# Optimization experiments

Measured on AMD Instinct MI355X. Metric: run time of the kernel, lower is better.

The kernel has to match this reference:

```python
import jax, jax.numpy as jnp
import numpy as np
from jax import lax

N_STATES = 128
N_NL = 64
N_IN = 64
N_OUT = 32
N_SYS = 16
FILT = 24
GAMMA = 1e-3
Q_VAL = 10.0
BETA = 1e5
EPS = 1e-3
BATCH = 131072


def setup_inputs() -> dict:
    key = jax.random.key(0)
    ks = jax.random.split(key, 11)
    std = 0.1
    return {
        "inpt": jax.random.normal(ks[0], (BATCH, N_IN), jnp.float32),
        "state": jax.random.normal(ks[1], (BATCH, N_STATES), jnp.float32),
        "X": jax.random.normal(ks[2], (2 * N_STATES + N_NL, 2 * N_STATES + N_NL), jnp.float32) * std,
        "Y1": jax.random.normal(ks[3], (N_STATES, N_STATES), jnp.float32) * std,
        "X3": jax.random.normal(ks[4], (N_OUT, N_OUT), jnp.float32) * std,
        "Y3": jax.random.normal(ks[5], (N_OUT, N_OUT), jnp.float32) * std,
        "Z3": jax.random.normal(ks[6], (abs(N_IN - N_OUT), N_OUT), jnp.float32) * std,
        "B2": jax.random.normal(ks[7], (N_STATES, N_IN), jnp.float32) * std,
        "C2": jax.random.normal(ks[8], (N_OUT, N_STATES), jnp.float32) * std,
        "D21": jax.random.normal(ks[9], (N_OUT, N_NL), jnp.float32) * std,
        "D12": jax.random.normal(ks[10], (N_NL, N_IN), jnp.float32) * std,
    }


def _derived(X, Y1, X3, Y3, Z3, B2, C2, D21, D12):
    # set_model_param(): build contracting REN matrices from free params.
    s = min(N_IN, N_OUT)  # = N_OUT here
    Q = -Q_VAL * jnp.eye(N_OUT, dtype=X.dtype)
    m = N_IN - N_SYS
    R_diag = jnp.concatenate([
        BETA * jnp.ones(N_SYS), GAMMA * jnp.ones(FILT - 1),
        jnp.array([BETA]), GAMMA * jnp.ones(m - FILT)]).astype(X.dtype)
    R = jnp.diag(R_diag)
    I_s = jnp.eye(s, dtype=X.dtype)
    M = X3.T @ X3 + Y3 - Y3.T + Z3.T @ Z3 + EPS * I_s
    Minv = jnp.linalg.inv(I_s + M)
    # n_outputs < n_inputs branch
    N = jnp.concatenate([Minv @ (I_s - M), -2.0 * Minv @ Z3.T], axis=1)  # [n_out, n_in]
    Lq = jnp.linalg.cholesky(-Q).T
    Lr = jnp.linalg.cholesky(R).T
    D22 = jnp.linalg.inv(Lq) @ N @ Lr  # [n_out, n_in]
    R_cal = R + D22.T @ Q @ D22
    R_cal_inv = jnp.linalg.inv(R_cal)
    C2_cal = (D22.T @ Q @ C2).T            # [n_states, n_in]
    D21_cal = (D22.T @ Q @ D21).T - D12    # [n_nl, n_in]
    vec_r = jnp.concatenate([C2_cal, D21_cal, B2], axis=0)
    psi_r = vec_r @ R_cal_inv @ vec_r.T
    vec_q = jnp.concatenate([C2.T, D21.T, jnp.zeros((N_STATES, N_OUT), X.dtype)], axis=0)
    psi_q = vec_q @ Q @ vec_q.T
    n = 2 * N_STATES + N_NL
    H = X.T @ X + EPS * jnp.eye(n, dtype=X.dtype) + psi_r - psi_q
    ns, nl = N_STATES, N_NL
    H11 = H[:ns, :ns]
    H21 = H[ns:ns + nl, :ns]
    H22 = H[ns:ns + nl, ns:ns + nl]
    H31 = H[ns + nl:, :ns]
    H32 = H[ns + nl:, ns:ns + nl]
    H33 = H[ns + nl:, ns + nl:]
    Fm = H31
    B1 = H32
    E = 0.5 * (H11 + H33 + Y1 - Y1.T)
    Lam = 0.5 * jnp.diag(H22)
    D11 = -jnp.tril(H22, k=-1)  # strictly lower triangular
    C1 = -H21
    return Fm, B1, E, Lam, C1, D11, D22


def _ren_forward(inpt, state, X, Y1, X3, Y3, Z3, B2, C2, D21, D12):
    Fm, B1, E, Lam, C1, D11, D22 = _derived(X, Y1, X3, Y3, Z3, B2, C2, D21, D12)
    B = state.shape[0]
    # precompute the state/input contribution to every nonlinearity row
    a = state @ C1.T + inpt @ D12.T  # [B, n_nl] (bias = 0, bias=False)

    def step(w, xs):
        i, a_col, d11_row, lam = xs
        v = a_col + w @ d11_row                 # forward substitution: D11 strictly lower
        w = w.at[:, i].set(jnp.tanh(v / lam))
        return w, None

    w0 = jnp.zeros((B, N_NL), dtype=state.dtype)
    xs = (jnp.arange(N_NL), a.T, D11, Lam)
    w, _ = lax.scan(step, w0, xs)

    E_x_ = state @ Fm.T + w @ B1.T + inpt @ B2.T
    state_plus = E_x_ @ jnp.linalg.inv(E).T
    output = state @ C2.T + w @ D21.T + inpt @ D22.T
    return output, state_plus


def reference(inpt, state, X, Y1, X3, Y3, Z3, B2, C2, D21, D12):
    return _ren_forward(inpt, state, X, Y1, X3, Y3, Z3, B2, C2, D21, D12)
```

## Files before the change

### kernel.cpp

```cpp
#include <hip/hip_runtime.h>
#include <math.h>

#define BATCH 131072
#define NTOT 320

typedef __attribute__((ext_vector_type(8))) short short8;
typedef __attribute__((ext_vector_type(4))) float f32x4;

#define WS_D22   0
#define WS_VR    2048
#define WS_T     22528
#define WS_H     43008
#define WS_E     145408
#define WS_EINV  161792
#define WS_WEXT  178176
#define WS_D11   210944
#define WS_ILAM  215040
#define WS_BFU   215104
#define U_WATH 0
#define U_WATL 16384
#define U_WOT  32768
#define U_WSPH 40960
#define U_WSPL 73728
#define WS_M    (WS_H)
#define WS_A32M (WS_H + 1024)
#define WS_RC   (WS_H + 2048)

__device__ inline unsigned short f2bf(float x){
    unsigned u = __builtin_bit_cast(unsigned, x);
    u += 0x7FFFu + ((u >> 16) & 1u);
    return (unsigned short)(u >> 16);
}
__device__ inline float bf2f(unsigned short h){
    unsigned u = ((unsigned)h) << 16;
    return __builtin_bit_cast(float, u);
}
__device__ inline float r_diag(int j) {
    return (j < 16 || j == 39) ? 100000.0f : 0.001f;
}

__global__ __launch_bounds__(256) void k_der1a(
    const float* __restrict__ X3, const float* __restrict__ Y3,
    const float* __restrict__ Z3, float* __restrict__ ws)
{
    int idx = blockIdx.x*256 + threadIdx.x;
    if (idx >= 1024) return;
    int i = idx >> 5, j = idx & 31;
    float s = 0.f;
    for (int k = 0; k < 32; ++k)
        s += X3[k*32+i]*X3[k*32+j] + Z3[k*32+i]*Z3[k*32+j];
    s += Y3[i*32+j] - Y3[j*32+i];
    if (i == j) s += 0.001f;
    ws[WS_M + idx]    = s;
    ws[WS_A32M + idx] = s + (i == j ? 1.f : 0.f);
}

__global__ __launch_bounds__(1024) void k_gj32(float* __restrict__ ws)
{
    __shared__ float A32[32*33];
    const int t = threadIdx.x;
    const int i = t >> 5, j = t & 31;
    A32[i*33+j] = ws[WS_A32M + i*32 + j];
    __syncthreads();
    for (int k = 0; k < 32; ++k) {
        float ip = 1.f / A32[k*33+k];
        float f  = A32[i*33+k];
        float pj = A32[k*33+j];
        __syncthreads();
        float nv;
        if (i == k) nv = (j == k) ? ip : pj*ip;
        else        nv = (j == k) ? (-f*ip) : (A32[i*33+j] - f*ip*pj);
        A32[i*33+j] = nv;
        __syncthreads();
    }
    ws[WS_A32M + i*32 + j] = A32[i*33+j];
}

__global__ __launch_bounds__(512) void k_der1b(
    const float* __restrict__ Z3, float* __restrict__ ws)
{
    __shared__ float Ms[1024], Mi[1024], D22s[2048];
    const int t = threadIdx.x;
    for (int idx = t; idx < 1024; idx += 512) {
        Ms[idx] = ws[WS_M + idx];
        Mi[idx] = ws[WS_A32M + idx];
    }
    __syncthreads();
    for (int idx = t; idx < 2048; idx += 512) {
        int i = idx >> 6, j = idx & 63;
        float s = 0.f;
        if (j < 32) {
            for (int k = 0; k < 32; ++k) {
                float im = (k == j ? 1.f : 0.f) - Ms[k*32+j];
                s += Mi[i*32+k]*im;
            }
        } else {
            int jj = j - 32;
            for (int k = 0; k < 32; ++k) s += Mi[i*32+k]*Z3[jj*32+k];
            s *= -2.f;
        }
        float d22 = s * sqrtf(r_diag(j)) * 0.31622776601683794f;
        D22s[idx] = d22;
        ws[WS_D22 + idx] = d22;
    }
    __syncthreads();
    for (int idx = t; idx < 4096; idx += 512) {
        int i = idx >> 6, j = idx & 63;
        float s = 0.f;
        for (int k = 0; k < 32; ++k) s += D22s[k*64+i]*D22s[k*64+j];
        float v = -10.f*s;
        if (i == j) v += r_diag(i);
        ws[WS_RC + idx] = v;
    }
}

__global__ __launch_bounds__(256) void k_gj64(float* __restrict__ ws)
{
    __shared__ float piv[2][64];
    __shared__ float fcol[2][64];
    __shared__ float ipd[2];
    const int t = threadIdx.x;
    const int q = t >> 6;
    const int i = t & 63;
    const int c0 = q*16;

    float Ar[16];
    {
        const float* Rin = ws + WS_RC + i*64 + c0;
        #pragma unroll
        for (int jj = 0; jj < 4; ++jj) {
            float4 v = *(const float4*)(Rin + jj*4);
            Ar[jj*4+0]=v.x; Ar[jj*4+1]=v.y; Ar[jj*4+2]=v.z; Ar[jj*4+3]=v.w;
        }
    }

    for (int k = 0; k < 64; ++k) {
        const int b  = k & 1;
        const int kq = k >> 4;
        const int kj = k & 15;

        float f_own = Ar[0];
        #pragma unroll
        for (int jj = 1; jj < 16; ++jj) f_own = (jj == kj) ? Ar[jj] : f_own;

        if (q == kq) fcol[b][i] = f_own;
        if (i == k) {
            #pragma unroll
            for (int jj = 0; jj < 4; ++jj) {
                float4 v;
                v.x = Ar[jj*4+0] + ((q==kq && jj*4+0==kj) ? 1.f : 0.f);
                v.y = Ar[jj*4+1] + ((q==kq && jj*4+1==kj) ? 1.f : 0.f);
                v.z = Ar[jj*4+2] + ((q==kq && jj*4+2==kj) ? 1.f : 0.f);
                v.w = Ar[jj*4+3] + ((q==kq && jj*4+3==kj) ? 1.f : 0.f);
                *(float4*)(&piv[b][c0 + jj*4]) = v;
            }
            if (q == kq) ipd[b] = 1.f / f_own;
        }
        __syncthreads();

        const float ipv = ipd[b];
        if (i == k) {
            #pragma unroll
            for (int jj = 0; jj < 16; ++jj)
                Ar[jj] = (q==kq && jj==kj) ? ipv : Ar[jj]*ipv;
        } else {
            const float g = fcol[b][i] * ipv;
            #pragma unroll
            for (int jj = 0; jj < 4; ++jj) {
                float4 pv = *(const float4*)(&piv[b][c0 + jj*4]);
                Ar[jj*4+0] -= g*pv.x;
                Ar[jj*4+1] -= g*pv.y;
                Ar[jj*4+2] -= g*pv.z;
                Ar[jj*4+3] -= g*pv.w;
            }
        }
    }

    {
        float* Rout = ws + WS_RC + i*64 + c0;
        #pragma unroll
        for (int jj = 0; jj < 4; ++jj) {
            float4 v;
            v.x=Ar[jj*4+0]; v.y=Ar[jj*4+1]; v.z=Ar[jj*4+2]; v.w=Ar[jj*4+3];
            *(float4*)(Rout + jj*4) = v;
        }
    }
}

__global__ __launch_bounds__(256) void k_vecr(
    const float* __restrict__ B2, const float* __restrict__ C2,
    const float* __restrict__ D21, const float* __restrict__ D12,
    float* __restrict__ ws)
{
    int idx = blockIdx.x*256 + threadIdx.x;
    if (idx >= 320*64) return;
    int i = idx >> 6, j = idx & 63;
    const float* D22 = ws + WS_D22;
    float v;
    if (i < 128) {
        float s = 0.f;
        for (int k = 0; k < 32; ++k) s += C2[k*128+i]*D22[k*64+j];
        v = -10.f*s;
    } else if (i < 192) {
        int ii = i - 128;
        float s = 0.f;
        for (int k = 0; k < 32; ++k) s += D21[k*64+ii]*D22[k*64+j];
        v = -10.f*s - D12[ii*64+j];
    } else {
        v = B2[(i-192)*64 + j];
    }
    ws[WS_VR+idx] = v;
}

__global__ __launch_bounds__(256) void k_T(float* __restrict__ ws)
{
    int idx = blockIdx.x*256 + threadIdx.x;
    if (idx >= 320*64) return;
    int i = idx >> 6, j = idx & 63;
    const float* VR = ws + WS_VR + i*64;
    const float* RC = ws + WS_RC;
    float s = 0.f;
    for (int k = 0; k < 64; ++k) s += VR[k] * RC[k*64+j];
    ws[WS_T+idx] = s;
}

__global__ void k_H(const float* __restrict__ X, const float* __restrict__ C2,
                    const float* __restrict__ D21, float* __restrict__ ws)
{
    int idx = blockIdx.x*256 + threadIdx.x;
    if (idx >= NTOT*NTOT) return;
    int i = idx / NTOT, j = idx % NTOT;
    float s = (i == j) ? 0.001f : 0.f;
    for (int k = 0; k < NTOT; ++k) s += X[k*NTOT+i]*X[k*NTOT+j];
    const float* T  = ws + WS_T;
    const float* vr = ws + WS_VR;
    float s2 = 0.f;
    for (int k = 0; k < 64; ++k) s2 += T[i*64+k]*vr[j*64+k];
    s += s2;
    if (i < 192 && j < 192) {
        float s3 = 0.f;
        for (int k = 0; k < 32; ++k) {
            float qi = (i < 128) ? C2[k*128+i] : D21[k*64 + (i-128)];
            float qj = (j < 128) ? C2[k*128+j] : D21[k*64 + (j-128)];
            s3 += qi*qj;
        }
        s += 10.f*s3;
    }
    ws[WS_H + idx] = s;
}

__global__ void k_extract(const float* __restrict__ Y1, const float* __restrict__ C2,
                          const float* __restrict__ D21, const float* __restrict__ D12,
                          const float* __restrict__ B2, float* __restrict__ ws)
{
    const float* H = ws + WS_H;
    unsigned short* bfb = (unsigned short*)(ws + WS_BFU);
    int tid = blockIdx.x*blockDim.x + threadIdx.x;
    int nth = gridDim.x*blockDim.x;
    for (int idx = tid; idx < 128*128; idx += nth) {
        int i = idx >> 7, j = idx & 127;
        ws[WS_E+idx] = 0.5f*(H[i*320+j] + H[(192+i)*320 + 192+j] + Y1[i*128+j] - Y1[j*128+i]);
    }
    for (int i = tid; i < 64; i += nth)
        ws[WS_ILAM+i] = 2.0f / H[(128+i)*320 + 128+i];
    for (int idx = tid; idx < 64*64; idx += nth) {
        int i = idx >> 6, j = idx & 63;
        ws[WS_D11+idx] = (j < i) ? -H[(128+i)*320 + 128+j] : 0.f;
    }
    for (int idx = tid; idx < 128*256; idx += nth) {
        int m = idx >> 8, k = idx & 255;
        ws[WS_WEXT+idx] = (k < 192) ? H[(192+m)*320 + k] : B2[m*64 + (k-192)];
    }
    for (int idx = tid; idx < 64*256; idx += nth) {
        int j = idx >> 8, k = idx & 255;
        float v;
        if (k < 128)      v = -H[(128+j)*320 + k];
        else if (k < 192) v = 0.f;
        else              v = D12[j*64 + (k-192)];
        unsigned short hi = f2bf(v);
        bfb[U_WATH+idx] = hi;
        bfb[U_WATL+idx] = f2bf(v - bf2f(hi));
    }
    const float* D22 = ws + WS_D22;
    for (int idx = tid; idx < 32*256; idx += nth) {
        int c = idx >> 8, k = idx & 255;
        float v;
        if (k < 128)      v = C2[c*128+k];
        else if (k < 192) v = D21[c*64 + (k-128)];
        else              v = D22[c*64 + (k-192)];
        bfb[U_WOT+idx] = f2bf(v);
    }
}

__global__ __launch_bounds__(1024) void k_inv128(float* __restrict__ ws)
{
    __shared__ float piv[2][128];
    __shared__ float fcol[2][128];
    __shared__ float ipd[2];
    const int t = threadIdx.x;
    const int q = t >> 7;
    const int i = t & 127;
    const int c0 = q*16;

    float Ar[16];
    {
        const float* Ein = ws + WS_E + i*128 + c0;
        #pragma unroll
        for (int jj = 0; jj < 4; ++jj) {
            float4 v = *(const float4*)(Ein + jj*4);
            Ar[jj*4+0]=v.x; Ar[jj*4+1]=v.y; Ar[jj*4+2]=v.z; Ar[jj*4+3]=v.w;
        }
    }

    for (int k = 0; k < 128; ++k) {
        const int b  = k & 1;
        const int kq = k >> 4;
        const int kj = k & 15;

        float f_own = Ar[0];
        #pragma unroll
        for (int jj = 1; jj < 16; ++jj) f_own = (jj == kj) ? Ar[jj] : f_own;

        if (q == kq) fcol[b][i] = f_own;
        if (i == k) {
            #pragma unroll
            for (int jj = 0; jj < 4; ++jj) {
                float4 v;
                v.x = Ar[jj*4+0] + ((q==kq && jj*4+0==kj) ? 1.f : 0.f);
                v.y = Ar[jj*4+1] + ((q==kq && jj*4+1==kj) ? 1.f : 0.f);
                v.z = Ar[jj*4+2] + ((q==kq && jj*4+2==kj) ? 1.f : 0.f);
                v.w = Ar[jj*4+3] + ((q==kq && jj*4+3==kj) ? 1.f : 0.f);
                *(float4*)(&piv[b][c0 + jj*4]) = v;
            }
            if (q == kq) ipd[b] = 1.f / f_own;
        }
        __syncthreads();

        const float ipv = ipd[b];
        if (i == k) {
            #pragma unroll
            for (int jj = 0; jj < 16; ++jj)
                Ar[jj] = (q==kq && jj==kj) ? ipv : Ar[jj]*ipv;
        } else {
            const float g = fcol[b][i] * ipv;
            #pragma unroll
            for (int jj = 0; jj < 4; ++jj) {
                float4 pv = *(const float4*)(&piv[b][c0 + jj*4]);
                Ar[jj*4+0] -= g*pv.x;
                Ar[jj*4+1] -= g*pv.y;
                Ar[jj*4+2] -= g*pv.z;
                Ar[jj*4+3] -= g*pv.w;
            }
        }
    }

    {
        float* Eout = ws + WS_EINV + i*128 + c0;
        #pragma unroll
        for (int jj = 0; jj < 4; ++jj) {
            float4 v;
            v.x=Ar[jj*4+0]; v.y=Ar[jj*4+1]; v.z=Ar[jj*4+2]; v.w=Ar[jj*4+3];
            *(float4*)(Eout + jj*4) = v;
        }
    }
}

__global__ __launch_bounds__(256) void k_Wsp(float* __restrict__ ws)
{
    int i = blockIdx.x;
    int k = threadIdx.x;
    const float* Einv = ws + WS_EINV + i*128;
    const float* WexT = ws + WS_WEXT;
    unsigned short* bfb = (unsigned short*)(ws + WS_BFU);
    float s = 0.f;
    for (int m = 0; m < 128; ++m) s += Einv[m] * WexT[m*256 + k];
    unsigned short hi = f2bf(s);
    bfb[U_WSPH + i*256 + k] = hi;
    bfb[U_WSPL + i*256 + k] = f2bf(s - bf2f(hi));
}

__global__ __launch_bounds__(256, 4) void k_batch(
    const float* __restrict__ inpt, const float* __restrict__ state,
    const float* __restrict__ ws, float* __restrict__ out)
{
    __shared__ unsigned short zsh[64*256];
    __shared__ unsigned short D11t[64*64];
    const int t = threadIdx.x;
    const int row0 = blockIdx.x * 64;
    const unsigned short* bfb = (const unsigned short*)(ws + WS_BFU);

    for (int idx = t; idx < 64*16; idx += 256) {
        int r = idx >> 4, c = idx & 15;
        const float4* p = (const float4*)(state + (size_t)(row0+r)*128 + c*8);
        float4 f0 = p[0], f1 = p[1];
        short8 h;
        h[0]=(short)f2bf(f0.x); h[1]=(short)f2bf(f0.y); h[2]=(short)f2bf(f0.z); h[3]=(short)f2bf(f0.w);
        h[4]=(short)f2bf(f1.x); h[5]=(short)f2bf(f1.y); h[6]=(short)f2bf(f1.z); h[7]=(short)f2bf(f1.w);
        *(short8*)(&zsh[r*256 + ((c ^ (r&7)) << 3)]) = h;
    }
    for (int idx = t; idx < 64*8; idx += 256) {
        int r = idx >> 3, cl = idx & 7, c = 24 + cl;
        const float4* p = (const float4*)(inpt + (size_t)(row0+r)*64 + cl*8);
        float4 f0 = p[0], f1 = p[1];
        short8 h;
        h[0]=(short)f2bf(f0.x); h[1]=(short)f2bf(f0.y); h[2]=(short)f2bf(f0.z); h[3]=(short)f2bf(f0.w);
        h[4]=(short)f2bf(f1.x); h[5]=(short)f2bf(f1.y); h[6]=(short)f2bf(f1.z); h[7]=(short)f2bf(f1.w);
        *(short8*)(&zsh[r*256 + ((c ^ (r&7)) << 3)]) = h;
    }
    for (int idx = t; idx < 4096; idx += 256) {
        int j = idx >> 6, i = idx & 63;
        float v = (i == j) ? ws[WS_ILAM + j] : ws[WS_D11 + i*64 + j];
        D11t[idx] = f2bf(v);
    }
    __syncthreads();

    const int wv = t >> 6, lane = t & 63, lr = lane & 15, lk = lane >> 4;

    {
        const unsigned short* WATH = bfb + U_WATH;
        const unsigned short* WATL = bfb + U_WATL;
        f32x4 acc1[4] = {};
        const int ks1[6] = {0,1,2,3,6,7};
        #pragma unroll
        for (int s = 0; s < 6; ++s) {
            int ks = ks1[s];
            short8 bh = *(const short8*)(&WATH[(wv*16+lr)*256 + ks*32 + lk*8]);
            short8 bl = *(const short8*)(&WATL[(wv*16+lr)*256 + ks*32 + lk*8]);
            #pragma unroll
            for (int rt = 0; rt < 4; ++rt) {
                int row = rt*16 + lr, c = ks*4 + lk;
                short8 a = *(const short8*)(&zsh[row*256 + ((c ^ (row&7)) << 3)]);
                acc1[rt] = __builtin_amdgcn_mfma_f32_16x16x32_bf16(a, bh, acc1[rt], 0, 0, 0);
                acc1[rt] = __builtin_amdgcn_mfma_f32_16x16x32_bf16(a, bl, acc1[rt], 0, 0, 0);
            }
        }
        __syncthreads();
        const int ac = wv*16 + lr;
        const int cch = 16 + (ac >> 3), coff = ac & 7;
        #pragma unroll
        for (int rt = 0; rt < 4; ++rt)
            #pragma unroll
            for (int r = 0; r < 4; ++r) {
                int row = rt*16 + lk*4 + r;
                zsh[row*256 + ((cch ^ (row&7)) << 3) + coff] = f2bf(acc1[rt][r]);
            }
    }
    __syncthreads();

    {
        const int r  = wv*16 + (lane >> 2);
        const int qq = lane & 3;
        float acc[16];
        #pragma unroll
        for (int s = 0; s < 16; ++s) {
            int i = qq*16 + s;
            int cch = 16 + (i >> 3);
            acc[s] = bf2f(zsh[r*256 + ((cch ^ (r&7)) << 3) + (i & 7)]);
        }
        float wloc[16];
        #pragma unroll
        for (int j = 0; j < 64; ++j) {
            float diag = bf2f(D11t[j*64 + j]);
            float v = acc[j & 15];
            float x = v * diag;
            float e = __expf(2.f*x);
            float wc = 1.f - __fdividef(2.f, e + 1.f);
            int src = (lane & 0x3C) | (j >> 4);
            float wj = __shfl(wc, src, 64);
            if ((j >> 4) == qq) wloc[j & 15] = wj;
            #pragma unroll
            for (int s = 0; s < 16; ++s)
                acc[s] += wj * bf2f(D11t[j*64 + qq*16 + s]);
        }
        #pragma unroll
        for (int cc = 0; cc < 2; ++cc) {
            int ch = 16 + qq*2 + cc;
            short8 h;
            #pragma unroll
            for (int e2 = 0; e2 < 8; ++e2) h[e2] = (short)f2bf(wloc[cc*8 + e2]);
            *(short8*)(&zsh[r*256 + ((ch ^ (r&7)) << 3)]) = h;
        }
    }
    __syncthreads();

    {
        const unsigned short* WOT  = bfb + U_WOT;
        const unsigned short* WSPH = bfb + U_WSPH;
        const unsigned short* WSPL = bfb + U_WSPL;
        f32x4 acc[3][4] = {};
        const int nt = (wv < 2) ? 3 : 2;
        #pragma unroll
        for (int ks = 0; ks < 8; ++ks) {
            short8 afr[4];
            #pragma unroll
            for (int rt = 0; rt < 4; ++rt) {
                int row = rt*16 + lr, c = ks*4 + lk;
                afr[rt] = *(const short8*)(&zsh[row*256 + ((c ^ (row&7)) << 3)]);
            }
            #pragma unroll
            for (int tt = 0; tt < 3; ++tt) {
                if (tt < nt) {
                    int ct = wv + tt*4;
                    if (ct < 2) {
                        short8 b = *(const short8*)(&WOT[(ct*16+lr)*256 + ks*32 + lk*8]);
                        #pragma unroll
                        for (int rt = 0; rt < 4; ++rt)
                            acc[tt][rt] = __builtin_amdgcn_mfma_f32_16x16x32_bf16(afr[rt], b, acc[tt][rt], 0, 0, 0);
                    } else {
                        short8 bh = *(const short8*)(&WSPH[((ct-2)*16+lr)*256 + ks*32 + lk*8]);
                        short8 bl = *(const short8*)(&WSPL[((ct-2)*16+lr)*256 + ks*32 + lk*8]);
                        #pragma unroll
                        for (int rt = 0; rt < 4; ++rt) {
                            acc[tt][rt] = __builtin_amdgcn_mfma_f32_16x16x32_bf16(afr[rt], bh, acc[tt][rt], 0, 0, 0);
                            acc[tt][rt] = __builtin_amdgcn_mfma_f32_16x16x32_bf16(afr[rt], bl, acc[tt][rt], 0, 0, 0);
                        }
                    }
                }
            }
        }
        float* sp = out + (size_t)BATCH*32;
        #pragma unroll
        for (int tt = 0; tt < 3; ++tt) {
            if (tt < nt) {
                int ct = wv + tt*4;
                #pragma unroll
                for (int rt = 0; rt < 4; ++rt) {
                    int rowb = row0 + rt*16 + lk*4;
                    #pragma unroll
                    for (int r = 0; r < 4; ++r) {
                        float vv = acc[tt][rt][r];
                        if (ct < 2) out[(size_t)(rowb+r)*32  + ct*16 + lr]     = vv;
                        else        sp[(size_t)(rowb+r)*128 + (ct-2)*16 + lr] = vv;
                    }
                }
            }
        }
    }
}

extern "C" void kernel_launch(void* const* d_in, const int* in_sizes, int n_in,
                              void* d_out, int out_size, void* d_ws, size_t ws_size,
                              hipStream_t stream)
{
    const float* inpt  = (const float*)d_in[0];
    const float* state = (const float*)d_in[1];
    const float* X   = (const float*)d_in[2];
    const float* Y1  = (const float*)d_in[3];
    const float* X3  = (const float*)d_in[4];
    const float* Y3  = (const float*)d_in[5];
    const float* Z3  = (const float*)d_in[6];
    const float* B2  = (const float*)d_in[7];
    const float* C2  = (const float*)d_in[8];
    const float* D21 = (const float*)d_in[9];
    const float* D12 = (const float*)d_in[10];
    float* ws  = (float*)d_ws;
    float* out = (float*)d_out;

    k_der1a<<<4, 256, 0, stream>>>(X3, Y3, Z3, ws);
    k_gj32<<<1, 1024, 0, stream>>>(ws);
    k_der1b<<<1, 512, 0, stream>>>(Z3, ws);
    k_gj64<<<1, 256, 0, stream>>>(ws);
    k_vecr<<<80, 256, 0, stream>>>(B2, C2, D21, D12, ws);
    k_T<<<80, 256, 0, stream>>>(ws);
    k_H<<<(NTOT*NTOT + 255)/256, 256, 0, stream>>>(X, C2, D21, ws);
    k_extract<<<128, 256, 0, stream>>>(Y1, C2, D21, D12, B2, ws);
    k_inv128<<<1, 1024, 0, stream>>>(ws);
    k_Wsp<<<128, 256, 0, stream>>>(ws);
    k_batch<<<BATCH/64, 256, 0, stream>>>(inpt, state, ws, out);
}
```

Measured before the change: 315.6 us.

## Invert E by block Schur complement using two 64x64 Gauss-Jordan solves

Replaces the single-block 128x128 Gauss-Jordan inversion of E with a 2x2 block inversion. The top-left 64x64 block and the Schur complement are each inverted by a generalized 64x64 Gauss-Jordan kernel, and the remaining blocks are assembled by small matmul kernels. The aim is to shorten the serial pivot chain, which currently runs in a 1024-thread block that synchronizes at every step. The price is five extra kernel launches, scratch buffers placed in the now-unused H region, and a reliance on the top-left block being well conditioned without pivoting.

```diff
diff --git a/kernel.cpp b/kernel.cpp
--- a/kernel.cpp
+++ b/kernel.cpp
@@ -25,6 +25,11 @@
 #define WS_M    (WS_H)
 #define WS_A32M (WS_H + 1024)
 #define WS_RC   (WS_H + 2048)
+#define SC_AI   (WS_H)
+#define SC_P    (WS_H + 4096)
+#define SC_S    (WS_H + 8192)
+#define SC_Q    (WS_H + 12288)
+#define SC_R    (WS_H + 16384)
 
 __device__ inline unsigned short f2bf(float x){
     unsigned u = __builtin_bit_cast(unsigned, x);
@@ -114,7 +119,8 @@
     }
 }
 
-__global__ __launch_bounds__(256) void k_gj64(float* __restrict__ ws)
+__global__ __launch_bounds__(256) void kS_gj64g(float* __restrict__ ws,
+    int srcOff, int srcStride, int dstOff, int dstStride)
 {
     __shared__ float piv[2][64];
     __shared__ float fcol[2][64];
@@ -126,7 +132,7 @@
 
     float Ar[16];
     {
-        const float* Rin = ws + WS_RC + i*64 + c0;
+        const float* Rin = ws + srcOff + i*srcStride + c0;
         #pragma unroll
         for (int jj = 0; jj < 4; ++jj) {
             float4 v = *(const float4*)(Rin + jj*4);
@@ -177,7 +183,7 @@
     }
 
     {
-        float* Rout = ws + WS_RC + i*64 + c0;
+        float* Rout = ws + dstOff + i*dstStride + c0;
         #pragma unroll
         for (int jj = 0; jj < 4; ++jj) {
             float4 v;
@@ -292,77 +298,65 @@
     }
 }
 
-__global__ __launch_bounds__(1024) void k_inv128(float* __restrict__ ws)
-{
-    __shared__ float piv[2][128];
-    __shared__ float fcol[2][128];
-    __shared__ float ipd[2];
-    const int t = threadIdx.x;
-    const int q = t >> 7;
-    const int i = t & 127;
-    const int c0 = q*16;
-
-    float Ar[16];
-    {
-        const float* Ein = ws + WS_E + i*128 + c0;
-        #pragma unroll
-        for (int jj = 0; jj < 4; ++jj) {
-            float4 v = *(const float4*)(Ein + jj*4);
-            Ar[jj*4+0]=v.x; Ar[jj*4+1]=v.y; Ar[jj*4+2]=v.z; Ar[jj*4+3]=v.w;
-        }
-    }
-
-    for (int k = 0; k < 128; ++k) {
-        const int b  = k & 1;
-        const int kq = k >> 4;
-        const int kj = k & 15;
-
-        float f_own = Ar[0];
-        #pragma unroll
-        for (int jj = 1; jj < 16; ++jj) f_own = (jj == kj) ? Ar[jj] : f_own;
-
-        if (q == kq) fcol[b][i] = f_own;
-        if (i == k) {
-            #pragma unroll
-            for (int jj = 0; jj < 4; ++jj) {
-                float4 v;
-                v.x = Ar[jj*4+0] + ((q==kq && jj*4+0==kj) ? 1.f : 0.f);
-                v.y = Ar[jj*4+1] + ((q==kq && jj*4+1==kj) ? 1.f : 0.f);
-                v.z = Ar[jj*4+2] + ((q==kq && jj*4+2==kj) ? 1.f : 0.f);
-                v.w = Ar[jj*4+3] + ((q==kq && jj*4+3==kj) ? 1.f : 0.f);
-                *(float4*)(&piv[b][c0 + jj*4]) = v;
-            }
-            if (q == kq) ipd[b] = 1.f / f_own;
-        }
-        __syncthreads();
-
-        const float ipv = ipd[b];
-        if (i == k) {
-            #pragma unroll
-            for (int jj = 0; jj < 16; ++jj)
-                Ar[jj] = (q==kq && jj==kj) ? ipv : Ar[jj]*ipv;
-        } else {
-            const float g = fcol[b][i] * ipv;
-            #pragma unroll
-            for (int jj = 0; jj < 4; ++jj) {
-                float4 pv = *(const float4*)(&piv[b][c0 + jj*4]);
-                Ar[jj*4+0] -= g*pv.x;
-                Ar[jj*4+1] -= g*pv.y;
-                Ar[jj*4+2] -= g*pv.z;
-                Ar[jj*4+3] -= g*pv.w;
-            }
-        }
-    }
-
-    {
-        float* Eout = ws + WS_EINV + i*128 + c0;
-        #pragma unroll
-        for (int jj = 0; jj < 4; ++jj) {
-            float4 v;
-            v.x=Ar[jj*4+0]; v.y=Ar[jj*4+1]; v.z=Ar[jj*4+2]; v.w=Ar[jj*4+3];
-            *(float4*)(Eout + jj*4) = v;
-        }
-    }
+__global__ __launch_bounds__(256) void kS_P(float* __restrict__ ws)
+{
+    int idx = blockIdx.x*256 + threadIdx.x;
+    int i = idx >> 6, j = idx & 63;
+    const float* AI = ws + SC_AI + i*64;
+    const float* E  = ws + WS_E;
+    float s = 0.f;
+    for (int k = 0; k < 64; ++k) s += AI[k] * E[k*128 + 64 + j];
+    ws[SC_P + idx] = s;
+}
+__global__ __launch_bounds__(256) void kS_S(float* __restrict__ ws)
+{
+    int idx = blockIdx.x*256 + threadIdx.x;
+    int i = idx >> 6, j = idx & 63;
+    const float* E = ws + WS_E;
+    const float* C = E + (64+i)*128;
+    const float* P = ws + SC_P;
+    float s = E[(64+i)*128 + 64 + j];
+    for (int k = 0; k < 64; ++k) s -= C[k] * P[k*64 + j];
+    ws[SC_S + idx] = s;
+}
+__global__ __launch_bounds__(256) void kS_Q(float* __restrict__ ws)
+{
+    int idx = blockIdx.x*256 + threadIdx.x;
+    int i = idx >> 6, j = idx & 63;
+    const float* E = ws + WS_E;
+    const float* C = E + (64+i)*128;
+    const float* AI = ws + SC_AI;
+    float s = 0.f;
+    for (int k = 0; k < 64; ++k) s += C[k] * AI[k*64 + j];
+    ws[SC_Q + idx] = s;
+}
+__global__ __launch_bounds__(256) void kS_R(float* __restrict__ ws)
+{
+    int idx = blockIdx.x*256 + threadIdx.x;
+    int i = idx >> 6, j = idx & 63;
+    const float* Si = ws + SC_S + i*64;
+    const float* Q  = ws + SC_Q;
+    float s = 0.f;
+    for (int k = 0; k < 64; ++k) s += Si[k] * Q[k*64 + j];
+    ws[SC_R + idx] = s;
+    ws[WS_EINV + (64+i)*128 + j] = -s;
+}
+__global__ __launch_bounds__(256) void kS_TL(float* __restrict__ ws)
+{
+    int idx = blockIdx.x*256 + threadIdx.x;
+    int i = idx >> 6, j = idx & 63;
+    const float* P  = ws + SC_P + i*64;
+    const float* R2 = ws + SC_R;
+    const float* Si = ws + SC_S;
+    float s1 = ws[SC_AI + idx];
+    float s2 = 0.f;
+    for (int k = 0; k < 64; ++k) {
+        s1 += P[k] * R2[k*64 + j];
+        s2 += P[k] * Si[k*64 + j];
+    }
+    ws[WS_EINV + i*128 + j]        = s1;
+    ws[WS_EINV + i*128 + 64 + j]   = -s2;
+    ws[WS_EINV + (64+i)*128 + 64 + j] = Si[i*64 + j];
 }
 
 __global__ __launch_bounds__(256) void k_Wsp(float* __restrict__ ws)
@@ -559,12 +553,18 @@
     k_der1a<<<4, 256, 0, stream>>>(X3, Y3, Z3, ws);
     k_gj32<<<1, 1024, 0, stream>>>(ws);
     k_der1b<<<1, 512, 0, stream>>>(Z3, ws);
-    k_gj64<<<1, 256, 0, stream>>>(ws);
+    kS_gj64g<<<1, 256, 0, stream>>>(ws, WS_RC, 64, WS_RC, 64);
     k_vecr<<<80, 256, 0, stream>>>(B2, C2, D21, D12, ws);
     k_T<<<80, 256, 0, stream>>>(ws);
     k_H<<<(NTOT*NTOT + 255)/256, 256, 0, stream>>>(X, C2, D21, ws);
     k_extract<<<128, 256, 0, stream>>>(Y1, C2, D21, D12, B2, ws);
-    k_inv128<<<1, 1024, 0, stream>>>(ws);
+    kS_gj64g<<<1, 256, 0, stream>>>(ws, WS_E, 128, SC_AI, 64);
+    kS_P<<<16, 256, 0, stream>>>(ws);
+    kS_S<<<16, 256, 0, stream>>>(ws);
+    kS_gj64g<<<1, 256, 0, stream>>>(ws, SC_S, 64, SC_S, 64);
+    kS_Q<<<16, 256, 0, stream>>>(ws);
+    kS_R<<<16, 256, 0, stream>>>(ws);
+    kS_TL<<<16, 256, 0, stream>>>(ws);
     k_Wsp<<<128, 256, 0, stream>>>(ws);
     k_batch<<<BATCH/64, 256, 0, stream>>>(inpt, state, ws, out);
 }
```

Measured after the change: 299.3 us. -5.1%, faster.
